# Kernel tuning notes

Measured on AMD Instinct MI355X. Metric: run time of the kernel, lower is better.

Reference implementation:

```python
import jax, jax.numpy as jnp
import numpy as np

N_NODES = 100000
N_EDGES = 3200000
IN_CH = 128
HID = 64


def setup_inputs() -> dict:
    key = jax.random.key(0)
    k1, k2, k3, k4 = jax.random.split(key, 4)
    x = jax.random.normal(k1, (N_NODES, IN_CH), dtype=jnp.float32)
    edge_index = jax.random.randint(k2, (2, N_EDGES), 0, N_NODES, dtype=jnp.int64)
    W1 = jax.random.normal(k3, (IN_CH, HID), dtype=jnp.float32) * (1.0 / np.sqrt(IN_CH))
    b1 = jnp.zeros((HID,), dtype=jnp.float32)
    W2 = jax.random.normal(k4, (HID, HID), dtype=jnp.float32) * (1.0 / np.sqrt(HID))
    b2 = jnp.zeros((HID,), dtype=jnp.float32)
    return {"x": x, "edge_index": edge_index, "W1": W1, "b1": b1, "W2": W2, "b2": b2}


def _gcn_conv(x, W, b, src, dst, deg_inv_sqrt, n_nodes):
    # GCNConv with self-loops and symmetric normalization:
    # out_i = sum_{j->i} d_j^-1/2 d_i^-1/2 (x_j W) + d_i^-1 (x_i W) + b
    h = x @ W                                   # [N, out]
    norm = deg_inv_sqrt[src] * deg_inv_sqrt[dst]  # [E]
    agg = jax.ops.segment_sum(h[src] * norm[:, None], dst, num_segments=n_nodes)
    agg = agg + h * (deg_inv_sqrt * deg_inv_sqrt)[:, None]  # self-loop term
    return agg + b


def reference(x, edge_index, W1, b1, W2, b2):
    n = x.shape[0]
    src, dst = edge_index[0], edge_index[1]
    # degree including self-loop
    deg = jax.ops.segment_sum(jnp.ones_like(dst, dtype=x.dtype), dst, num_segments=n) + 1.0
    deg_inv_sqrt = jax.lax.rsqrt(deg)
    h = jax.nn.relu(_gcn_conv(x, W1, b1, src, dst, deg_inv_sqrt, n))
    h = jax.nn.relu(_gcn_conv(h, W2, b2, src, dst, deg_inv_sqrt, n))
    # AdaptiveAvgPool1d(1) over the node dim -> [HID]
    return jnp.mean(h, axis=0)
```

## Files before the change

### kernel.cpp

```cpp
#include <hip/hip_runtime.h>


#define CAP 8192
#define PA_T 4096

typedef float v2f __attribute__((vector_size(8)));

__device__ __forceinline__ void acc_fp8x8(uint2 w, v2f* acc) {
    acc[0] += __builtin_amdgcn_cvt_pk_f32_fp8((int)w.x, false);
    acc[1] += __builtin_amdgcn_cvt_pk_f32_fp8((int)w.x, true);
    acc[2] += __builtin_amdgcn_cvt_pk_f32_fp8((int)w.y, false);
    acc[3] += __builtin_amdgcn_cvt_pk_f32_fp8((int)w.y, true);
}
__device__ __forceinline__ unsigned f32x4_to_fp8(float a, float b, float c, float d) {
    int w = 0;
    w = __builtin_amdgcn_cvt_pk_fp8_f32(a, b, w, false);
    w = __builtin_amdgcn_cvt_pk_fp8_f32(c, d, w, true);
    return (unsigned)w;
}

__global__ __launch_bounds__(256)
void pass_a_kernel(const int* __restrict__ src, const int* __restrict__ dst,
                   int* __restrict__ bcur, unsigned* __restrict__ keys, int e, int nb) {
    __shared__ unsigned skeys[PA_T];
    __shared__ unsigned short sbkt[PA_T];
    __shared__ int hist[1024];
    __shared__ int base[1024];
    __shared__ int gbase[1024];
    __shared__ int curs[1024];
    __shared__ int wsum[4];

    const int tid = threadIdx.x;
    const int lane = tid & 63;
    const int wv = tid >> 6;
    const int e0 = blockIdx.x * PA_T;
    const int cnt = min(PA_T, e - e0);

    for (int i = tid; i < 1024; i += 256) hist[i] = 0;
    __syncthreads();

    for (int i = tid; i < cnt; i += 256) {
        int d = dst[e0 + i];
        atomicAdd(&hist[d >> 7], 1);
    }
    __syncthreads();

    {
        int t4 = tid * 4;
        int a0 = hist[t4], a1 = hist[t4 + 1], a2 = hist[t4 + 2], a3 = hist[t4 + 3];
        int tsum = a0 + a1 + a2 + a3;
        int inc = tsum;
        for (int off = 1; off < 64; off <<= 1) {
            int v = __shfl_up(inc, off);
            if (lane >= off) inc += v;
        }
        if (lane == 63) wsum[wv] = inc;
        __syncthreads();
        int wbase = 0;
#pragma unroll
        for (int w = 0; w < 4; ++w) wbase += (w < wv) ? wsum[w] : 0;
        int ex = wbase + inc - tsum;
        base[t4] = ex;
        base[t4 + 1] = ex + a0;
        base[t4 + 2] = ex + a0 + a1;
        base[t4 + 3] = ex + a0 + a1 + a2;
        curs[t4] = base[t4];
        curs[t4 + 1] = base[t4 + 1];
        curs[t4 + 2] = base[t4 + 2];
        curs[t4 + 3] = base[t4 + 3];
    }
    __syncthreads();

    for (int i = tid; i < cnt; i += 256) {
        int s = src[e0 + i], d = dst[e0 + i];
        int b = d >> 7;
        int pos = atomicAdd(&curs[b], 1);
        skeys[pos] = ((unsigned)s << 7) | (unsigned)(d & 127);
        sbkt[pos] = (unsigned short)b;
    }
    __syncthreads();

    for (int b = tid; b < nb; b += 256) {
        int c = hist[b];
        gbase[b] = c ? atomicAdd(&bcur[b], c) : 0;
    }
    __syncthreads();

    for (int i = tid; i < cnt; i += 256) {
        int b = sbkt[i];
        int gi = gbase[b] + (i - base[b]);
        keys[(size_t)b * CAP + gi] = skeys[i];
    }
}

__global__ __launch_bounds__(1024)
void bscan_kernel(const int* __restrict__ bcur, int* __restrict__ bbase,
                  int* __restrict__ rowptr, int nb, int n) {
    __shared__ int lds[1024];
    int t = threadIdx.x;
    int v = (t < nb) ? bcur[t] : 0;
    lds[t] = v;
    __syncthreads();
    for (int off = 1; off < 1024; off <<= 1) {
        int a = (t >= off) ? lds[t - off] : 0;
        __syncthreads();
        lds[t] += a;
        __syncthreads();
    }
    if (t < nb) bbase[t] = lds[t] - v;
    if (t == 1023) rowptr[n] = lds[1023];
}

__global__ __launch_bounds__(256)
void bucket_csr_kernel(const unsigned* __restrict__ keys, const int* __restrict__ bcur,
                       const int* __restrict__ bbase, float* __restrict__ dis,
                       int* __restrict__ rowptr, int* __restrict__ csr_src, int n) {
    __shared__ int ssrc[CAP];
    __shared__ int hist[128];
    __shared__ int curs[128];
    __shared__ int sc[256];

    const int tid = threadIdx.x;
    const int b = blockIdx.x;
    const int v0 = b << 7;
    const int nv = min(128, n - v0);
    const int ne = bcur[b];
    const int gb = bbase[b];
    const size_t kb = (size_t)b * CAP;

    if (tid < 128) hist[tid] = 0;
    __syncthreads();
    for (int i = tid; i < ne; i += 256) atomicAdd(&hist[keys[kb + i] & 127u], 1);
    __syncthreads();

    int hv = (tid < 128) ? hist[tid] : 0;
    sc[tid] = hv;
    __syncthreads();
    for (int off = 1; off < 128; off <<= 1) {
        int a = (tid >= off) ? sc[tid - off] : 0;
        __syncthreads();
        sc[tid] += a;
        __syncthreads();
    }
    if (tid < 128) {
        int ex = sc[tid] - hv;
        curs[tid] = ex;
        if (tid < nv) {
            rowptr[v0 + tid] = gb + ex;
            dis[v0 + tid] = rsqrtf((float)hv + 1.0f);
        }
    }
    __syncthreads();

    for (int i = tid; i < ne; i += 256) {
        unsigned k = keys[kb + i];
        int pos = atomicAdd(&curs[k & 127u], 1);
        ssrc[pos] = (int)((k >> 7) << 6);
    }
    __syncthreads();

    for (int i = tid; i < ne; i += 256) csr_src[gb + i] = ssrc[i];
}

template <int K, bool FP8_IN>
__global__ __launch_bounds__(256)
void gemm_kernel(const void* __restrict__ Av, const float* __restrict__ B,
                 const float* __restrict__ dis, unsigned char* __restrict__ H, int n) {
    constexpr int KP = K + 4;
    __shared__ float As[64 * KP];
    __shared__ float Bs[K * 64];
    const int tid = threadIdx.x;
    const int row0 = blockIdx.x * 64;

    constexpr int A4 = 64 * (K / 4);
    for (int idx = tid; idx < A4; idx += 256) {
        int row = idx / (K / 4);
        int c4  = idx % (K / 4);
        float4 v = make_float4(0.f, 0.f, 0.f, 0.f);
        int r = row0 + row;
        if (r < n) {
            if (FP8_IN) {
                unsigned w = *reinterpret_cast<const unsigned*>(
                    (const unsigned char*)Av + (size_t)r * K + c4 * 4);
                v2f lo = __builtin_amdgcn_cvt_pk_f32_fp8((int)w, false);
                v2f hi = __builtin_amdgcn_cvt_pk_f32_fp8((int)w, true);
                v = make_float4(lo[0], lo[1], hi[0], hi[1]);
            } else {
                v = *reinterpret_cast<const float4*>((const float*)Av + (size_t)r * K + c4 * 4);
            }
        }
        *reinterpret_cast<float4*>(&As[row * KP + c4 * 4]) = v;
    }
    constexpr int B4 = K * 16;
    for (int idx = tid; idx < B4; idx += 256) {
        int row = idx / 16, c4 = idx % 16;
        *reinterpret_cast<float4*>(&Bs[row * 64 + c4 * 4]) =
            *reinterpret_cast<const float4*>(B + row * 64 + c4 * 4);
    }
    __syncthreads();

    const int tr = tid >> 4;
    const int tc = tid & 15;
    float acc[4][4];
#pragma unroll
    for (int j = 0; j < 4; ++j)
#pragma unroll
        for (int i = 0; i < 4; ++i) acc[j][i] = 0.f;

    for (int k4 = 0; k4 < K / 4; ++k4) {
        float4 a[4], bq[4];
#pragma unroll
        for (int j = 0; j < 4; ++j)
            a[j] = *reinterpret_cast<const float4*>(&As[(tr * 4 + j) * KP + k4 * 4]);
#pragma unroll
        for (int kk = 0; kk < 4; ++kk)
            bq[kk] = *reinterpret_cast<const float4*>(&Bs[(k4 * 4 + kk) * 64 + tc * 4]);
#pragma unroll
        for (int kk = 0; kk < 4; ++kk) {
#pragma unroll
            for (int j = 0; j < 4; ++j) {
                float av = (kk == 0) ? a[j].x : (kk == 1) ? a[j].y : (kk == 2) ? a[j].z : a[j].w;
                acc[j][0] = fmaf(av, bq[kk].x, acc[j][0]);
                acc[j][1] = fmaf(av, bq[kk].y, acc[j][1]);
                acc[j][2] = fmaf(av, bq[kk].z, acc[j][2]);
                acc[j][3] = fmaf(av, bq[kk].w, acc[j][3]);
            }
        }
    }

#pragma unroll
    for (int j = 0; j < 4; ++j) {
        int r = row0 + tr * 4 + j;
        if (r < n) {
            float ds = dis[r];
            unsigned w = f32x4_to_fp8(acc[j][0] * ds, acc[j][1] * ds,
                                      acc[j][2] * ds, acc[j][3] * ds);
            *reinterpret_cast<unsigned*>(H + (size_t)r * 64 + tc * 4) = w;
        }
    }
}

template <bool WRITE_OUT>
__global__ __launch_bounds__(256)
void agg_kernel(const int* __restrict__ rowptr, const int* __restrict__ csr_src,
                const unsigned char* __restrict__ h, const float* __restrict__ dis,
                const float* __restrict__ bias,
                unsigned char* __restrict__ out, float* __restrict__ outsum,
                int n, int zoff, float inv_n) {
    const int tid = threadIdx.x;
    const int lane = tid & 63;
    const int o = lane >> 3;
    const int cl = lane & 7;
    const int wid = blockIdx.x * 4 + (tid >> 6);
    const int nw = gridDim.x * 4;
    const int ngroups = (n + 7) >> 3;

    float bl[8];
    {
        float4 b0 = *reinterpret_cast<const float4*>(bias + cl * 8);
        float4 b1 = *reinterpret_cast<const float4*>(bias + cl * 8 + 4);
        bl[0] = b0.x; bl[1] = b0.y; bl[2] = b0.z; bl[3] = b0.w;
        bl[4] = b1.x; bl[5] = b1.y; bl[6] = b1.z; bl[7] = b1.w;
    }
    float bsum[8];
#pragma unroll
    for (int k = 0; k < 8; ++k) bsum[k] = 0.f;

    for (int g = wid; g < ngroups; g += nw) {
        const int node = g * 8 + o;
        const bool live = node < n;
        const int nc = live ? node : n - 1;
        const int rp0 = rowptr[nc];
        const int rp1 = rowptr[nc + 1];
        const int deg = live ? (rp1 - rp0) : 0;
        const float ds = dis[nc];

        v2f acc[4];
        {
            int so = live ? node * 64 : zoff;
            uint2 hw = *reinterpret_cast<const uint2*>(h + (size_t)(unsigned)so + cl * 8);
            acc[0] = __builtin_amdgcn_cvt_pk_f32_fp8((int)hw.x, false);
            acc[1] = __builtin_amdgcn_cvt_pk_f32_fp8((int)hw.x, true);
            acc[2] = __builtin_amdgcn_cvt_pk_f32_fp8((int)hw.y, false);
            acc[3] = __builtin_amdgcn_cvt_pk_f32_fp8((int)hw.y, true);
        }

        int md = deg;
        md = max(md, __shfl_xor(md, 8));
        md = max(md, __shfl_xor(md, 16));
        md = max(md, __shfl_xor(md, 32));

        if (md > 0) {
            int o0 = (0 < deg) ? csr_src[rp0]     : zoff;
            int o1 = (1 < deg) ? csr_src[rp0 + 1] : zoff;
            int o2 = (2 < deg) ? csr_src[rp0 + 2] : zoff;
            int o3 = (3 < deg) ? csr_src[rp0 + 3] : zoff;
            for (int it = 0; it < md; it += 4) {
                uint2 g0 = *reinterpret_cast<const uint2*>(h + (size_t)(unsigned)o0 + cl * 8);
                uint2 g1 = *reinterpret_cast<const uint2*>(h + (size_t)(unsigned)o1 + cl * 8);
                uint2 g2 = *reinterpret_cast<const uint2*>(h + (size_t)(unsigned)o2 + cl * 8);
                uint2 g3 = *reinterpret_cast<const uint2*>(h + (size_t)(unsigned)o3 + cl * 8);
                int c0 = csr_src[rp0 + it + 4];
                int c1 = csr_src[rp0 + it + 5];
                int c2 = csr_src[rp0 + it + 6];
                int c3 = csr_src[rp0 + it + 7];
                o0 = (it + 4 < deg) ? c0 : zoff;
                o1 = (it + 5 < deg) ? c1 : zoff;
                o2 = (it + 6 < deg) ? c2 : zoff;
                o3 = (it + 7 < deg) ? c3 : zoff;
                acc_fp8x8(g0, acc);
                acc_fp8x8(g1, acc);
                acc_fp8x8(g2, acc);
                acc_fp8x8(g3, acc);
            }
        }

        float val[8];
#pragma unroll
        for (int k = 0; k < 4; ++k) {
            val[2 * k]     = fmaxf(fmaf(acc[k][0], ds, bl[2 * k]), 0.f);
            val[2 * k + 1] = fmaxf(fmaf(acc[k][1], ds, bl[2 * k + 1]), 0.f);
        }
        if (WRITE_OUT) {
            if (live) {
                unsigned w0 = f32x4_to_fp8(val[0], val[1], val[2], val[3]);
                unsigned w1 = f32x4_to_fp8(val[4], val[5], val[6], val[7]);
                *reinterpret_cast<uint2*>(out + (size_t)node * 64 + cl * 8) = make_uint2(w0, w1);
            }
        } else {
            if (live) {
#pragma unroll
                for (int k = 0; k < 8; ++k) bsum[k] += val[k];
            }
        }
    }

    if (!WRITE_OUT) {
        __shared__ float lds[4][64];
#pragma unroll
        for (int k = 0; k < 8; ++k) {
            float v = bsum[k];
            v += __shfl_xor(v, 8);
            v += __shfl_xor(v, 16);
            v += __shfl_xor(v, 32);
            bsum[k] = v;
        }
        const int wv = tid >> 6;
        if (o == 0) {
#pragma unroll
            for (int k = 0; k < 8; ++k) lds[wv][cl * 8 + k] = bsum[k];
        }
        __syncthreads();
        if (tid < 64) {
            float s = lds[0][tid] + lds[1][tid] + lds[2][tid] + lds[3][tid];
            atomicAdd(&outsum[tid], s * inv_n);
        }
    }
}

extern "C" void kernel_launch(void* const* d_in, const int* in_sizes, int n_in,
                              void* d_out, int out_size, void* d_ws, size_t ws_size,
                              hipStream_t stream) {
    const float* x  = (const float*)d_in[0];
    const int*   ei = (const int*)d_in[1];
    const float* W1 = (const float*)d_in[2];
    const float* b1 = (const float*)d_in[3];
    const float* W2 = (const float*)d_in[4];
    const float* b2 = (const float*)d_in[5];

    const int n = in_sizes[0] / 128;
    const int e = in_sizes[1] / 2;
    const int* src = ei;
    const int* dst = ei + e;
    const int nb = (n + 127) >> 7;

    char* ws = (char*)d_ws;
    size_t off = 0;
    auto alloc = [&](size_t bytes) { void* p = ws + off; off = (off + bytes + 255) & ~(size_t)255; return p; };
    unsigned* keys = (unsigned*)alloc((size_t)nb * CAP * 4);
    int*   bcur    = (int*)  alloc((size_t)nb * 4);
    int*   bbase   = (int*)  alloc((size_t)nb * 4);
    float* dis     = (float*)alloc((size_t)n * 4);
    int*   rowptr  = (int*)  alloc((size_t)(n + 1) * 4);
    int*   csr_src = (int*)  alloc(((size_t)e + 64) * 4);
    unsigned char* bufA = (unsigned char*)alloc((size_t)(n + 1) * 64);
    unsigned char* bufB = (unsigned char*)alloc((size_t)(n + 1) * 64);

    hipMemsetAsync(bcur, 0, (size_t)nb * 4, stream);
    hipMemsetAsync(d_out, 0, 64 * sizeof(float), stream);
    hipMemsetAsync(bufA + (size_t)n * 64, 0, 64, stream);

    const int pa_blocks = (e + PA_T - 1) / PA_T;
    pass_a_kernel<<<pa_blocks, 256, 0, stream>>>(src, dst, bcur, keys, e, nb);
    bscan_kernel<<<1, 1024, 0, stream>>>(bcur, bbase, rowptr, nb, n);
    bucket_csr_kernel<<<nb, 256, 0, stream>>>(keys, bcur, bbase, dis, rowptr, csr_src, n);

    const int gblocks = (n + 63) / 64;
    const int zoff = n * 64;
    const int agg_blocks = 1563;
    gemm_kernel<128, false><<<gblocks, 256, 0, stream>>>(x, W1, dis, bufA, n);
    agg_kernel<true><<<agg_blocks, 256, 0, stream>>>(rowptr, csr_src, bufA, dis, b1,
                                                     bufB, nullptr, n, zoff, 0.f);
    gemm_kernel<64, true><<<gblocks, 256, 0, stream>>>(bufB, W2, dis, bufA, n);
    agg_kernel<false><<<agg_blocks, 256, 0, stream>>>(rowptr, csr_src, bufA, dis, b2,
                                                      nullptr, (float*)d_out, n, zoff, 1.0f / (float)n);
}
```

Baseline: 266.8 us.

## Split fp8 feature buffers into column halves and aggregate each half separately

```diff
diff --git a/kernel.cpp b/kernel.cpp
--- a/kernel.cpp
+++ b/kernel.cpp
@@ -155,7 +155,7 @@
     for (int i = tid; i < ne; i += 256) {
         unsigned k = keys[kb + i];
         int pos = atomicAdd(&curs[k & 127u], 1);
-        ssrc[pos] = (int)((k >> 7) << 6);
+        ssrc[pos] = (int)((k >> 7) << 5);
     }
     __syncthreads();
 
@@ -164,8 +164,9 @@
 
 template <int K, bool FP8_IN>
 __global__ __launch_bounds__(256)
-void gemm_kernel(const void* __restrict__ Av, const float* __restrict__ B,
-                 const float* __restrict__ dis, unsigned char* __restrict__ H, int n) {
+void gemm_kernel(const void* __restrict__ Av_lo, const void* __restrict__ Av_hi,
+                 const float* __restrict__ B, const float* __restrict__ dis,
+                 unsigned char* __restrict__ Hlo, unsigned char* __restrict__ Hhi, int n) {
     constexpr int KP = K + 4;
     __shared__ float As[64 * KP];
     __shared__ float Bs[K * 64];
@@ -180,13 +181,15 @@
         int r = row0 + row;
         if (r < n) {
             if (FP8_IN) {
-                unsigned w = *reinterpret_cast<const unsigned*>(
-                    (const unsigned char*)Av + (size_t)r * K + c4 * 4);
+                const unsigned char* p = (c4 < 8)
+                    ? ((const unsigned char*)Av_lo + (size_t)r * 32 + c4 * 4)
+                    : ((const unsigned char*)Av_hi + (size_t)r * 32 + (c4 - 8) * 4);
+                unsigned w = *reinterpret_cast<const unsigned*>(p);
                 v2f lo = __builtin_amdgcn_cvt_pk_f32_fp8((int)w, false);
                 v2f hi = __builtin_amdgcn_cvt_pk_f32_fp8((int)w, true);
                 v = make_float4(lo[0], lo[1], hi[0], hi[1]);
             } else {
-                v = *reinterpret_cast<const float4*>((const float*)Av + (size_t)r * K + c4 * 4);
+                v = *reinterpret_cast<const float4*>((const float*)Av_lo + (size_t)r * K + c4 * 4);
             }
         }
         *reinterpret_cast<float4*>(&As[row * KP + c4 * 4]) = v;
@@ -235,30 +238,32 @@
             float ds = dis[r];
             unsigned w = f32x4_to_fp8(acc[j][0] * ds, acc[j][1] * ds,
                                       acc[j][2] * ds, acc[j][3] * ds);
-            *reinterpret_cast<unsigned*>(H + (size_t)r * 64 + tc * 4) = w;
+            unsigned char* p = (tc < 8) ? (Hlo + (size_t)r * 32 + tc * 4)
+                                        : (Hhi + (size_t)r * 32 + (tc - 8) * 4);
+            *reinterpret_cast<unsigned*>(p) = w;
         }
     }
 }
 
 template <bool WRITE_OUT>
 __global__ __launch_bounds__(256)
-void agg_kernel(const int* __restrict__ rowptr, const int* __restrict__ csr_src,
-                const unsigned char* __restrict__ h, const float* __restrict__ dis,
-                const float* __restrict__ bias,
-                unsigned char* __restrict__ out, float* __restrict__ outsum,
-                int n, int zoff, float inv_n) {
+void agg_half_kernel(const int* __restrict__ rowptr, const int* __restrict__ csr_src,
+                     const unsigned char* __restrict__ h, const float* __restrict__ dis,
+                     const float* __restrict__ bias32,
+                     unsigned char* __restrict__ out, float* __restrict__ outsum32,
+                     int n, int zoff, float inv_n) {
     const int tid = threadIdx.x;
     const int lane = tid & 63;
-    const int o = lane >> 3;
-    const int cl = lane & 7;
+    const int o = lane >> 2;
+    const int cl = lane & 3;
     const int wid = blockIdx.x * 4 + (tid >> 6);
     const int nw = gridDim.x * 4;
-    const int ngroups = (n + 7) >> 3;
+    const int ngroups = (n + 15) >> 4;
 
     float bl[8];
     {
-        float4 b0 = *reinterpret_cast<const float4*>(bias + cl * 8);
-        float4 b1 = *reinterpret_cast<const float4*>(bias + cl * 8 + 4);
+        float4 b0 = *reinterpret_cast<const float4*>(bias32 + cl * 8);
+        float4 b1 = *reinterpret_cast<const float4*>(bias32 + cl * 8 + 4);
         bl[0] = b0.x; bl[1] = b0.y; bl[2] = b0.z; bl[3] = b0.w;
         bl[4] = b1.x; bl[5] = b1.y; bl[6] = b1.z; bl[7] = b1.w;
     }
@@ -267,7 +272,7 @@
     for (int k = 0; k < 8; ++k) bsum[k] = 0.f;
 
     for (int g = wid; g < ngroups; g += nw) {
-        const int node = g * 8 + o;
+        const int node = g * 16 + o;
         const bool live = node < n;
         const int nc = live ? node : n - 1;
         const int rp0 = rowptr[nc];
@@ -277,7 +282,7 @@
 
         v2f acc[4];
         {
-            int so = live ? node * 64 : zoff;
+            int so = live ? node * 32 : zoff;
             uint2 hw = *reinterpret_cast<const uint2*>(h + (size_t)(unsigned)so + cl * 8);
             acc[0] = __builtin_amdgcn_cvt_pk_f32_fp8((int)hw.x, false);
             acc[1] = __builtin_amdgcn_cvt_pk_f32_fp8((int)hw.x, true);
@@ -286,32 +291,29 @@
         }
 
         int md = deg;
+        md = max(md, __shfl_xor(md, 4));
         md = max(md, __shfl_xor(md, 8));
         md = max(md, __shfl_xor(md, 16));
         md = max(md, __shfl_xor(md, 32));
 
         if (md > 0) {
-            int o0 = (0 < deg) ? csr_src[rp0]     : zoff;
-            int o1 = (1 < deg) ? csr_src[rp0 + 1] : zoff;
-            int o2 = (2 < deg) ? csr_src[rp0 + 2] : zoff;
-            int o3 = (3 < deg) ? csr_src[rp0 + 3] : zoff;
-            for (int it = 0; it < md; it += 4) {
-                uint2 g0 = *reinterpret_cast<const uint2*>(h + (size_t)(unsigned)o0 + cl * 8);
-                uint2 g1 = *reinterpret_cast<const uint2*>(h + (size_t)(unsigned)o1 + cl * 8);
-                uint2 g2 = *reinterpret_cast<const uint2*>(h + (size_t)(unsigned)o2 + cl * 8);
-                uint2 g3 = *reinterpret_cast<const uint2*>(h + (size_t)(unsigned)o3 + cl * 8);
-                int c0 = csr_src[rp0 + it + 4];
-                int c1 = csr_src[rp0 + it + 5];
-                int c2 = csr_src[rp0 + it + 6];
-                int c3 = csr_src[rp0 + it + 7];
-                o0 = (it + 4 < deg) ? c0 : zoff;
-                o1 = (it + 5 < deg) ? c1 : zoff;
-                o2 = (it + 6 < deg) ? c2 : zoff;
-                o3 = (it + 7 < deg) ? c3 : zoff;
-                acc_fp8x8(g0, acc);
-                acc_fp8x8(g1, acc);
-                acc_fp8x8(g2, acc);
-                acc_fp8x8(g3, acc);
+            int ofs[8];
+#pragma unroll
+            for (int k = 0; k < 8; ++k)
+                ofs[k] = (k < deg) ? csr_src[rp0 + k] : zoff;
+            for (int it = 0; it < md; it += 8) {
+                uint2 gv[8];
+#pragma unroll
+                for (int k = 0; k < 8; ++k)
+                    gv[k] = *reinterpret_cast<const uint2*>(h + (size_t)(unsigned)ofs[k] + cl * 8);
+                int nx[8];
+#pragma unroll
+                for (int k = 0; k < 8; ++k) nx[k] = csr_src[rp0 + it + 8 + k];
+#pragma unroll
+                for (int k = 0; k < 8; ++k)
+                    ofs[k] = (it + 8 + k < deg) ? nx[k] : zoff;
+#pragma unroll
+                for (int k = 0; k < 8; ++k) acc_fp8x8(gv[k], acc);
             }
         }
 
@@ -325,7 +327,7 @@
             if (live) {
                 unsigned w0 = f32x4_to_fp8(val[0], val[1], val[2], val[3]);
                 unsigned w1 = f32x4_to_fp8(val[4], val[5], val[6], val[7]);
-                *reinterpret_cast<uint2*>(out + (size_t)node * 64 + cl * 8) = make_uint2(w0, w1);
+                *reinterpret_cast<uint2*>(out + (size_t)node * 32 + cl * 8) = make_uint2(w0, w1);
             }
         } else {
             if (live) {
@@ -336,10 +338,11 @@
     }
 
     if (!WRITE_OUT) {
-        __shared__ float lds[4][64];
+        __shared__ float lds[4][32];
 #pragma unroll
         for (int k = 0; k < 8; ++k) {
             float v = bsum[k];
+            v += __shfl_xor(v, 4);
             v += __shfl_xor(v, 8);
             v += __shfl_xor(v, 16);
             v += __shfl_xor(v, 32);
@@ -351,9 +354,9 @@
             for (int k = 0; k < 8; ++k) lds[wv][cl * 8 + k] = bsum[k];
         }
         __syncthreads();
-        if (tid < 64) {
+        if (tid < 32) {
             float s = lds[0][tid] + lds[1][tid] + lds[2][tid] + lds[3][tid];
-            atomicAdd(&outsum[tid], s * inv_n);
+            atomicAdd(&outsum32[tid], s * inv_n);
         }
     }
 }
@@ -382,13 +385,16 @@
     int*   bbase   = (int*)  alloc((size_t)nb * 4);
     float* dis     = (float*)alloc((size_t)n * 4);
     int*   rowptr  = (int*)  alloc((size_t)(n + 1) * 4);
-    int*   csr_src = (int*)  alloc(((size_t)e + 64) * 4);
-    unsigned char* bufA = (unsigned char*)alloc((size_t)(n + 1) * 64);
-    unsigned char* bufB = (unsigned char*)alloc((size_t)(n + 1) * 64);
+    int*   csr_src = (int*)  alloc(((size_t)e + 256) * 4);
+    unsigned char* bufA_lo = (unsigned char*)alloc((size_t)(n + 1) * 32);
+    unsigned char* bufA_hi = (unsigned char*)alloc((size_t)(n + 1) * 32);
+    unsigned char* bufB_lo = (unsigned char*)alloc((size_t)(n + 1) * 32);
+    unsigned char* bufB_hi = (unsigned char*)alloc((size_t)(n + 1) * 32);
 
     hipMemsetAsync(bcur, 0, (size_t)nb * 4, stream);
     hipMemsetAsync(d_out, 0, 64 * sizeof(float), stream);
-    hipMemsetAsync(bufA + (size_t)n * 64, 0, 64, stream);
+    hipMemsetAsync(bufA_lo + (size_t)n * 32, 0, 32, stream);
+    hipMemsetAsync(bufA_hi + (size_t)n * 32, 0, 32, stream);
 
     const int pa_blocks = (e + PA_T - 1) / PA_T;
     pass_a_kernel<<<pa_blocks, 256, 0, stream>>>(src, dst, bcur, keys, e, nb);
@@ -396,12 +402,18 @@
     bucket_csr_kernel<<<nb, 256, 0, stream>>>(keys, bcur, bbase, dis, rowptr, csr_src, n);
 
     const int gblocks = (n + 63) / 64;
-    const int zoff = n * 64;
+    const int zoff = n * 32;
     const int agg_blocks = 1563;
-    gemm_kernel<128, false><<<gblocks, 256, 0, stream>>>(x, W1, dis, bufA, n);
-    agg_kernel<true><<<agg_blocks, 256, 0, stream>>>(rowptr, csr_src, bufA, dis, b1,
-                                                     bufB, nullptr, n, zoff, 0.f);
-    gemm_kernel<64, true><<<gblocks, 256, 0, stream>>>(bufB, W2, dis, bufA, n);
-    agg_kernel<false><<<agg_blocks, 256, 0, stream>>>(rowptr, csr_src, bufA, dis, b2,
-                                                      nullptr, (float*)d_out, n, zoff, 1.0f / (float)n);
-}
+    float* outsum = (float*)d_out;
+
+    gemm_kernel<128, false><<<gblocks, 256, 0, stream>>>(x, nullptr, W1, dis, bufA_lo, bufA_hi, n);
+    agg_half_kernel<true><<<agg_blocks, 256, 0, stream>>>(rowptr, csr_src, bufA_lo, dis, b1,
+                                                          bufB_lo, nullptr, n, zoff, 0.f);
+    agg_half_kernel<true><<<agg_blocks, 256, 0, stream>>>(rowptr, csr_src, bufA_hi, dis, b1 + 32,
+                                                          bufB_hi, nullptr, n, zoff, 0.f);
+    gemm_kernel<64, true><<<gblocks, 256, 0, stream>>>(bufB_lo, bufB_hi, W2, dis, bufA_lo, bufA_hi, n);
+    agg_half_kernel<false><<<agg_blocks, 256, 0, stream>>>(rowptr, csr_src, bufA_lo, dis, b2,
+                                                           nullptr, outsum, n, zoff, 1.0f / (float)n);
+    agg_half_kernel<false><<<agg_blocks, 256, 0, stream>>>(rowptr, csr_src, bufA_hi, dis, b2 + 32,
+                                                           nullptr, outsum + 32, n, zoff, 1.0f / (float)n);
+}
```

Result: slower. 303.2 us (+13.6%).
